# Performance work log

Measured on AMD Instinct MI355X. Metric: run time of the kernel, lower is better.

The kernel has to match this reference:

```python
import jax, jax.numpy as jnp
import numpy as np

LOG2 = float(np.log(2.0))

def ssp(x):
    # schnetpack shifted softplus
    return jax.nn.softplus(x) - LOG2

def gather_neighbors(x, neighbors):
    # x: [B, A, F], neighbors: [B, A, N] int -> [B, A, N, F]
    B, A, N = neighbors.shape
    flat = neighbors.reshape(B, A * N)
    g = jnp.take_along_axis(x, flat[..., None], axis=1)
    return g.reshape(B, A, N, x.shape[-1])

def setup_inputs() -> dict:
    key = jax.random.key(0)
    ks = jax.random.split(key, 6)
    B, A, N, n_in, h = 32, 512, 256, 256, 128
    positions = jax.random.normal(ks[0], (B, A, 3), dtype=jnp.float32) * 3.0
    representation = jax.random.normal(ks[1], (B, A, n_in), dtype=jnp.float32)
    # neighbors guaranteed != self index to avoid zero distances
    off = jax.random.randint(ks[2], (B, A, N), 1, A)
    neighbors = (jnp.arange(A, dtype=jnp.int64)[None, :, None] + off.astype(jnp.int64)) % A
    nbh_mask = jnp.ones((B, A, N), dtype=jnp.float32)
    atom_mask = jnp.ones((B, A), dtype=jnp.float32)
    W1 = jax.random.normal(ks[3], (n_in, h), dtype=jnp.float32) / np.sqrt(n_in)
    b1 = jnp.zeros((h,), dtype=jnp.float32)
    W2 = jax.random.normal(ks[4], (h, 2), dtype=jnp.float32) / np.sqrt(h)
    b2 = jnp.zeros((2,), dtype=jnp.float32)
    return {"positions": positions, "representation": representation,
            "neighbors": neighbors, "nbh_mask": nbh_mask, "atom_mask": atom_mask,
            "W1": W1, "b1": b1, "W2": W2, "b2": b2}

def reference(positions, representation, neighbors, nbh_mask, atom_mask, W1, b1, W2, b2):
    # atom-wise MLP contributions: [B, A, 2]
    contrib = ssp(representation @ W1 + b1) @ W2 + b2

    # pairwise vectors/distances (neighbor - center): [B, A, N, 3], [B, A, N]
    pos_j = gather_neighbors(positions, neighbors)
    dist_vecs = pos_j - positions[:, :, None, :]
    distances = jnp.sqrt(jnp.sum(dist_vecs * dist_vecs, axis=-1))

    # gather neighbor contributions: [B, A, N, 2]
    nc = gather_neighbors(contrib, neighbors)
    nc1 = nc[..., 0]
    nc2 = nc[..., 1]

    # atomic dipoles: masked neighbor sum of dist_vecs * nc1 -> [B, A, 3]
    m = nbh_mask[..., None]
    atomic_dipoles = jnp.sum(dist_vecs * nc1[..., None] * m, axis=2)

    # distance-weighted fields
    masked_dist = distances ** 3 * nbh_mask + (1.0 - nbh_mask)
    nbh_fields = dist_vecs * nc2[..., None] / masked_dist[..., None]
    atomic_fields = jnp.sum(nbh_fields * m, axis=2)  # [B, A, 3]

    # normalize fields (guard tiny norms)
    field_norm = jnp.linalg.norm(atomic_fields, axis=-1, keepdims=True)
    field_norm = field_norm + (field_norm < 1e-10).astype(atomic_fields.dtype)
    atomic_fields = atomic_fields / field_norm

    # symmetric outer product: [B, A, 3, 3]
    ap = atomic_dipoles[..., None] * atomic_fields[:, :, None, :]
    atomic_polar = 0.5 * (ap + jnp.swapaxes(ap, -1, -2))

    # masked sum over atoms -> [B, 3, 3]
    global_polar = jnp.sum(atomic_polar * atom_mask[:, :, None, None], axis=1)
    return global_polar
```

## Files before the change

kernel.cpp:

```cpp
#include <hip/hip_runtime.h>
#include <math.h>

#define BATCH 32
#define NATOM 512
#define NNBH  256
#define NIN   256
#define NH    128

typedef __attribute__((ext_vector_type(8))) short bf16x8;
typedef __attribute__((ext_vector_type(4))) float f32x4;

__device__ __forceinline__ short f2bf(float f) {
    union { float f; unsigned u; } v; v.f = f;
    unsigned r = v.u + 0x7FFFu + ((v.u >> 16) & 1u);
    return (short)(r >> 16);
}

__global__ __launch_bounds__(256) void pack_w1(const float* __restrict__ W1,
                                               short* __restrict__ W1p) {
    int t = blockIdx.x * 256 + threadIdx.x;
    int h    = t & 7;
    int lane = (t >> 3) & 63;
    int n    = (t >> 9) & 7;
    int kb   = t >> 12;
    int k = kb * 32 + (lane >> 4) * 8 + h;
    int j = n * 16 + (lane & 15);
    W1p[t] = f2bf(W1[k * NH + j]);
}

__global__ __launch_bounds__(256) void mlp_mfma(
    const float* __restrict__ rep,
    const short* __restrict__ W1p,
    const float* __restrict__ b1,
    const float* __restrict__ W2,
    const float* __restrict__ b2,
    float* __restrict__ contrib)
{
    const int lane = threadIdx.x & 63;
    const int wave = threadIdx.x >> 6;
    const int rowBase = blockIdx.x * 64 + wave * 16;
    const int r0 = lane & 15;
    const int kg = lane >> 4;

    f32x4 acc[8];
    #pragma unroll
    for (int n = 0; n < 8; ++n) acc[n] = (f32x4){0.f, 0.f, 0.f, 0.f};

    #pragma unroll
    for (int kb = 0; kb < 8; ++kb) {
        const float* ap = rep + (size_t)(rowBase + r0) * NIN + kb * 32 + kg * 8;
        const float4 a0 = *(const float4*)ap;
        const float4 a1 = *(const float4*)(ap + 4);
        bf16x8 af;
        af[0] = f2bf(a0.x); af[1] = f2bf(a0.y); af[2] = f2bf(a0.z); af[3] = f2bf(a0.w);
        af[4] = f2bf(a1.x); af[5] = f2bf(a1.y); af[6] = f2bf(a1.z); af[7] = f2bf(a1.w);

        const short* bp = W1p + ((size_t)kb * 8 * 64 + lane) * 8;
        #pragma unroll
        for (int n = 0; n < 8; ++n) {
            bf16x8 bfr = *(const bf16x8*)(bp + (size_t)n * 64 * 8);
            acc[n] = __builtin_amdgcn_mfma_f32_16x16x32_bf16(af, bfr, acc[n], 0, 0, 0);
        }
    }

    float b1v[8], w2c0[8], w2c1[8];
    #pragma unroll
    for (int n = 0; n < 8; ++n) {
        const int j = n * 16 + (lane & 15);
        b1v[n] = b1[j];
        const float2 w2 = *(const float2*)(W2 + j * 2);
        w2c0[n] = w2.x; w2c1[n] = w2.y;
    }

    float c0[4], c1[4];
    #pragma unroll
    for (int reg = 0; reg < 4; ++reg) {
        float s0 = 0.f, s1 = 0.f;
        #pragma unroll
        for (int n = 0; n < 8; ++n) {
            const float z = acc[n][reg] + b1v[n];
            const float hv = fmaxf(z, 0.f) + log1pf(expf(-fabsf(z))) - 0.6931471805599453f;
            s0 = fmaf(hv, w2c0[n], s0);
            s1 = fmaf(hv, w2c1[n], s1);
        }
        c0[reg] = s0; c1[reg] = s1;
    }

    #pragma unroll
    for (int m = 8; m >= 1; m >>= 1) {
        #pragma unroll
        for (int reg = 0; reg < 4; ++reg) {
            c0[reg] += __shfl_xor(c0[reg], m, 64);
            c1[reg] += __shfl_xor(c1[reg], m, 64);
        }
    }

    if ((lane & 15) == 0) {
        const float bb0 = b2[0], bb1 = b2[1];
        #pragma unroll
        for (int reg = 0; reg < 4; ++reg) {
            const int row = rowBase + (lane >> 4) * 4 + reg;
            contrib[(size_t)row * 2 + 0] = c0[reg] + bb0;
            contrib[(size_t)row * 2 + 1] = c1[reg] + bb1;
        }
    }
}

__global__ __launch_bounds__(256) void pair_kernel(
    const float* __restrict__ positions,
    const int*   __restrict__ neighbors,
    const float* __restrict__ nbh_mask,
    const float* __restrict__ atom_mask,
    const float* __restrict__ contrib,
    float* __restrict__ partials)
{
    const int tid  = threadIdx.x;
    const int wave = tid >> 6;
    const int lane = tid & 63;
    const int atom = blockIdx.x * 4 + wave;
    const int b = atom >> 9;
    const int a = atom & (NATOM - 1);

    const float* posB = positions + (size_t)b * NATOM * 3;
    const float* ctrB = contrib   + (size_t)b * NATOM * 2;
    const float px = posB[a * 3 + 0];
    const float py = posB[a * 3 + 1];
    const float pz = posB[a * 3 + 2];
    const size_t nbase = (size_t)atom * NNBH;

    float dipx = 0.f, dipy = 0.f, dipz = 0.f;
    float fx = 0.f, fy = 0.f, fz = 0.f;

    const int4   idx4 = *(const int4*)(neighbors + nbase + lane * 4);
    const float4 m4   = *(const float4*)(nbh_mask + nbase + lane * 4);
    const int   idxs[4] = {idx4.x, idx4.y, idx4.z, idx4.w};
    const float ms[4]   = {m4.x, m4.y, m4.z, m4.w};

    #pragma unroll
    for (int i = 0; i < 4; ++i) {
        const int idx = idxs[i];
        const float m = ms[i];
        const float qx = posB[idx * 3 + 0];
        const float qy = posB[idx * 3 + 1];
        const float qz = posB[idx * 3 + 2];
        const float2 nc = *(const float2*)(ctrB + idx * 2);
        const float dx = qx - px, dy = qy - py, dz = qz - pz;
        const float d2 = dx * dx + dy * dy + dz * dz;
        const float dist = sqrtf(d2);
        const float md = dist * d2 * m + (1.f - m);
        const float nc1 = nc.x * m;
        const float nc2 = nc.y * m / md;
        dipx = fmaf(dx, nc1, dipx);
        dipy = fmaf(dy, nc1, dipy);
        dipz = fmaf(dz, nc1, dipz);
        fx = fmaf(dx, nc2, fx);
        fy = fmaf(dy, nc2, fy);
        fz = fmaf(dz, nc2, fz);
    }

    #pragma unroll
    for (int off = 32; off >= 1; off >>= 1) {
        dipx += __shfl_down(dipx, off, 64);
        dipy += __shfl_down(dipy, off, 64);
        dipz += __shfl_down(dipz, off, 64);
        fx   += __shfl_down(fx,   off, 64);
        fy   += __shfl_down(fy,   off, 64);
        fz   += __shfl_down(fz,   off, 64);
    }

    __shared__ float sw[4][9];
    if (lane == 0) {
        float norm = sqrtf(fx * fx + fy * fy + fz * fz);
        norm += (norm < 1e-10f) ? 1.f : 0.f;
        const float inv = 1.f / norm;
        const float f0 = fx * inv, f1 = fy * inv, f2 = fz * inv;
        const float am = atom_mask[(size_t)b * NATOM + a];
        const float d0 = dipx, d1 = dipy, d2v = dipz;
        sw[wave][0] = d0 * f0 * am;
        sw[wave][1] = 0.5f * (d0 * f1 + d1 * f0) * am;
        sw[wave][2] = 0.5f * (d0 * f2 + d2v * f0) * am;
        sw[wave][3] = 0.5f * (d1 * f0 + d0 * f1) * am;
        sw[wave][4] = d1 * f1 * am;
        sw[wave][5] = 0.5f * (d1 * f2 + d2v * f1) * am;
        sw[wave][6] = 0.5f * (d2v * f0 + d0 * f2) * am;
        sw[wave][7] = 0.5f * (d2v * f1 + d1 * f2) * am;
        sw[wave][8] = d2v * f2 * am;
    }
    __syncthreads();
    if (tid < 9) {
        partials[(size_t)blockIdx.x * 9 + tid] =
            sw[0][tid] + sw[1][tid] + sw[2][tid] + sw[3][tid];
    }
}

__global__ __launch_bounds__(128) void reduce_kernel(
    const float* __restrict__ partials,
    float* __restrict__ out)
{
    __shared__ float s[128][9];
    const int b = blockIdx.x;
    const int t = threadIdx.x;
    const float* p = partials + (size_t)b * 128 * 9;
    #pragma unroll
    for (int i = 0; i < 9; ++i) s[t][i] = p[(size_t)t * 9 + i];
    __syncthreads();
    if (t < 9) {
        float acc = 0.f;
        #pragma unroll 16
        for (int i = 0; i < 128; ++i) acc += s[i][t];
        out[(size_t)b * 9 + t] = acc;
    }
}

extern "C" void kernel_launch(void* const* d_in, const int* in_sizes, int n_in,
                              void* d_out, int out_size, void* d_ws, size_t ws_size,
                              hipStream_t stream) {
    const float* positions = (const float*)d_in[0];
    const float* rep       = (const float*)d_in[1];
    const int*   neighbors = (const int*)d_in[2];
    const float* nbh_mask  = (const float*)d_in[3];
    const float* atom_mask = (const float*)d_in[4];
    const float* W1        = (const float*)d_in[5];
    const float* b1        = (const float*)d_in[6];
    const float* W2        = (const float*)d_in[7];
    const float* b2        = (const float*)d_in[8];
    float* out = (float*)d_out;

    float* contrib  = (float*)d_ws;
    float* partials = contrib + (size_t)BATCH * NATOM * 2;
    short* W1p      = (short*)(partials + 4096 * 9);

    const int nRows = BATCH * NATOM;

    pack_w1<<<128, 256, 0, stream>>>(W1, W1p);
    mlp_mfma<<<nRows / 64, 256, 0, stream>>>(rep, W1p, b1, W2, b2, contrib);
    pair_kernel<<<nRows / 4, 256, 0, stream>>>(positions, neighbors, nbh_mask, atom_mask,
                                               contrib, partials);
    reduce_kernel<<<BATCH, 128, 0, stream>>>(partials, out);
}
```

Baseline: 39.76 us.

## Split MLP N dimension across waves with LDS-staged bf16 A tile

```diff
diff --git a/kernel.cpp b/kernel.cpp
--- a/kernel.cpp
+++ b/kernel.cpp
@@ -28,7 +28,7 @@
     W1p[t] = f2bf(W1[k * NH + j]);
 }
 
-__global__ __launch_bounds__(256) void mlp_mfma(
+__global__ __launch_bounds__(512, 4) void mlp_mfma(
     const float* __restrict__ rep,
     const short* __restrict__ W1p,
     const float* __restrict__ b1,
@@ -36,40 +36,53 @@
     const float* __restrict__ b2,
     float* __restrict__ contrib)
 {
-    const int lane = threadIdx.x & 63;
-    const int wave = threadIdx.x >> 6;
-    const int rowBase = blockIdx.x * 64 + wave * 16;
+    __shared__ short sA[32][264];
+    __shared__ float part[4][32][2];
+
+    const int tid    = threadIdx.x;
+    const int lane   = tid & 63;
+    const int wave   = tid >> 6;
+    const int rstrip = wave & 1;
+    const int npair  = wave >> 1;
+    const int rowBase = blockIdx.x * 32;
     const int r0 = lane & 15;
     const int kg = lane >> 4;
 
-    f32x4 acc[8];
-    #pragma unroll
-    for (int n = 0; n < 8; ++n) acc[n] = (f32x4){0.f, 0.f, 0.f, 0.f};
+    {
+        const int r  = tid >> 4;
+        const int c0 = (tid & 15) * 16;
+        const float4* src = (const float4*)(rep + (size_t)(rowBase + r) * NIN + c0);
+        const float4 v0 = src[0], v1 = src[1], v2 = src[2], v3 = src[3];
+        bf16x8 h0, h1;
+        h0[0] = f2bf(v0.x); h0[1] = f2bf(v0.y); h0[2] = f2bf(v0.z); h0[3] = f2bf(v0.w);
+        h0[4] = f2bf(v1.x); h0[5] = f2bf(v1.y); h0[6] = f2bf(v1.z); h0[7] = f2bf(v1.w);
+        h1[0] = f2bf(v2.x); h1[1] = f2bf(v2.y); h1[2] = f2bf(v2.z); h1[3] = f2bf(v2.w);
+        h1[4] = f2bf(v3.x); h1[5] = f2bf(v3.y); h1[6] = f2bf(v3.z); h1[7] = f2bf(v3.w);
+        *(bf16x8*)&sA[r][c0]     = h0;
+        *(bf16x8*)&sA[r][c0 + 8] = h1;
+    }
+    __syncthreads();
+
+    f32x4 acc[2];
+    acc[0] = (f32x4){0.f, 0.f, 0.f, 0.f};
+    acc[1] = (f32x4){0.f, 0.f, 0.f, 0.f};
 
     #pragma unroll
     for (int kb = 0; kb < 8; ++kb) {
-        const float* ap = rep + (size_t)(rowBase + r0) * NIN + kb * 32 + kg * 8;
-        const float4 a0 = *(const float4*)ap;
-        const float4 a1 = *(const float4*)(ap + 4);
-        bf16x8 af;
-        af[0] = f2bf(a0.x); af[1] = f2bf(a0.y); af[2] = f2bf(a0.z); af[3] = f2bf(a0.w);
-        af[4] = f2bf(a1.x); af[5] = f2bf(a1.y); af[6] = f2bf(a1.z); af[7] = f2bf(a1.w);
-
-        const short* bp = W1p + ((size_t)kb * 8 * 64 + lane) * 8;
-        #pragma unroll
-        for (int n = 0; n < 8; ++n) {
-            bf16x8 bfr = *(const bf16x8*)(bp + (size_t)n * 64 * 8);
-            acc[n] = __builtin_amdgcn_mfma_f32_16x16x32_bf16(af, bfr, acc[n], 0, 0, 0);
-        }
-    }
-
-    float b1v[8], w2c0[8], w2c1[8];
-    #pragma unroll
-    for (int n = 0; n < 8; ++n) {
-        const int j = n * 16 + (lane & 15);
-        b1v[n] = b1[j];
-        const float2 w2 = *(const float2*)(W2 + j * 2);
-        w2c0[n] = w2.x; w2c1[n] = w2.y;
+        const bf16x8 af = *(const bf16x8*)&sA[rstrip * 16 + r0][kb * 32 + kg * 8];
+        const bf16x8 bf0 = *(const bf16x8*)(W1p + ((size_t)(kb * 8 + npair * 2 + 0) * 64 + lane) * 8);
+        const bf16x8 bf1 = *(const bf16x8*)(W1p + ((size_t)(kb * 8 + npair * 2 + 1) * 64 + lane) * 8);
+        acc[0] = __builtin_amdgcn_mfma_f32_16x16x32_bf16(af, bf0, acc[0], 0, 0, 0);
+        acc[1] = __builtin_amdgcn_mfma_f32_16x16x32_bf16(af, bf1, acc[1], 0, 0, 0);
+    }
+
+    float b1v[2], w20[2], w21[2];
+    #pragma unroll
+    for (int nn = 0; nn < 2; ++nn) {
+        const int j = (npair * 2 + nn) * 16 + r0;
+        b1v[nn] = b1[j];
+        const float2 w = *(const float2*)(W2 + j * 2);
+        w20[nn] = w.x; w21[nn] = w.y;
     }
 
     float c0[4], c1[4];
@@ -77,11 +90,11 @@
     for (int reg = 0; reg < 4; ++reg) {
         float s0 = 0.f, s1 = 0.f;
         #pragma unroll
-        for (int n = 0; n < 8; ++n) {
-            const float z = acc[n][reg] + b1v[n];
+        for (int nn = 0; nn < 2; ++nn) {
+            const float z = acc[nn][reg] + b1v[nn];
             const float hv = fmaxf(z, 0.f) + log1pf(expf(-fabsf(z))) - 0.6931471805599453f;
-            s0 = fmaf(hv, w2c0[n], s0);
-            s1 = fmaf(hv, w2c1[n], s1);
+            s0 = fmaf(hv, w20[nn], s0);
+            s1 = fmaf(hv, w21[nn], s1);
         }
         c0[reg] = s0; c1[reg] = s1;
     }
@@ -95,14 +108,21 @@
         }
     }
 
-    if ((lane & 15) == 0) {
-        const float bb0 = b2[0], bb1 = b2[1];
+    if (r0 == 0) {
         #pragma unroll
         for (int reg = 0; reg < 4; ++reg) {
-            const int row = rowBase + (lane >> 4) * 4 + reg;
-            contrib[(size_t)row * 2 + 0] = c0[reg] + bb0;
-            contrib[(size_t)row * 2 + 1] = c1[reg] + bb1;
+            const int lr = rstrip * 16 + kg * 4 + reg;
+            part[npair][lr][0] = c0[reg];
+            part[npair][lr][1] = c1[reg];
         }
+    }
+    __syncthreads();
+
+    if (tid < 64) {
+        const int r = tid >> 1;
+        const int c = tid & 1;
+        const float s = part[0][r][c] + part[1][r][c] + part[2][r][c] + part[3][r][c] + b2[c];
+        contrib[(size_t)(rowBase + r) * 2 + c] = s;
     }
 }
 
@@ -233,7 +253,7 @@
     const int nRows = BATCH * NATOM;
 
     pack_w1<<<128, 256, 0, stream>>>(W1, W1p);
-    mlp_mfma<<<nRows / 64, 256, 0, stream>>>(rep, W1p, b1, W2, b2, contrib);
+    mlp_mfma<<<nRows / 32, 512, 0, stream>>>(rep, W1p, b1, W2, b2, contrib);
     pair_kernel<<<nRows / 4, 256, 0, stream>>>(positions, neighbors, nbh_mask, atom_mask,
                                                contrib, partials);
     reduce_kernel<<<BATCH, 128, 0, stream>>>(partials, out);
```

Result: faster. 37.67 us (-5.2%).
